# Optimization experiments

Hardware: AMD Instinct MI355X
Metric: run time of the kernel (lower is better)

Reference implementation:

```python
import jax, jax.numpy as jnp
import numpy as np

NUM_NODES = 100000
NUM_RELATIONS = 16
HIDDEN = 64
NUM_LAYERS = 3
NUM_EDGES = 1600000


def setup_inputs() -> dict:
    key = jax.random.key(0)
    ks = jax.random.split(key, 6)
    edge_index = jax.random.randint(ks[0], (2, NUM_EDGES), 0, NUM_NODES, dtype=jnp.int64 if jax.config.jax_enable_x64 else jnp.int32)
    edge_type = jax.random.randint(ks[1], (NUM_EDGES,), 0, NUM_RELATIONS, dtype=edge_index.dtype)
    scale = 1.0 / np.sqrt(HIDDEN)
    node_emb = jax.random.normal(ks[2], (NUM_NODES, HIDDEN), dtype=jnp.float32) * scale
    # Per-layer relation weights [L, R, d, h], root weights [L, d, h], bias [L, h]
    W = jax.random.normal(ks[3], (NUM_LAYERS, NUM_RELATIONS, HIDDEN, HIDDEN), dtype=jnp.float32) * scale
    W_root = jax.random.normal(ks[4], (NUM_LAYERS, HIDDEN, HIDDEN), dtype=jnp.float32) * scale
    bias = jnp.zeros((NUM_LAYERS, HIDDEN), dtype=jnp.float32)
    return {"edge_index": edge_index, "edge_type": edge_type,
            "node_emb": node_emb, "W": W, "W_root": W_root, "bias": bias}


def _rgcn_layer(x, src, dst, et, Wr, Wroot, b):
    # PyG RGCNConv: out_i = W_root x_i + b + sum_r (1/|N_r(i)|) sum_{j in N_r(i)} W_r x_j
    N, d = x.shape
    R = Wr.shape[0]
    # Transform all nodes by every relation weight: [R, N, h] (dense grouped GEMM)
    xW = jnp.einsum('nd,rdh->rnh', x, Wr)
    m = xW[et, src]                      # [E, h] per-edge messages (gather)
    seg = dst * R + et                   # joint (dst, relation) segment id
    counts = jax.ops.segment_sum(jnp.ones((m.shape[0],), dtype=x.dtype), seg, num_segments=N * R)
    norm = 1.0 / jnp.maximum(counts, 1.0)
    m = m * norm[seg][:, None]           # per-relation mean normalization
    agg = jax.ops.segment_sum(m, dst, num_segments=N)  # scatter-add over dst
    return agg + x @ Wroot + b


def reference(edge_index, edge_type, node_emb, W, W_root, bias):
    src, dst = edge_index[0], edge_index[1]
    x = node_emb  # note: Embedding.max_norm only applies on index lookups; .weight used raw here
    n_layers = W.shape[0]
    for i in range(n_layers):
        x = _rgcn_layer(x, src, dst, edge_type, W[i], W_root[i], bias[i])
        if i < n_layers - 1:
            x = jax.nn.relu(x)
    return x
```

## Files before the change

### kernel.cpp

```cpp
#include <hip/hip_runtime.h>


#define HID   64
#define NREL  16
#define KD    1088
#define NPB   16
#define NPW   2
#define LSTR  1096

#define NBKT  1024
#define BSH   7
#define FB    2048
#define CAPB  4096
#define CHA   8192

typedef __attribute__((ext_vector_type(8))) short bf16x8;
typedef __attribute__((ext_vector_type(4))) float f32x4;
typedef unsigned short us16;
typedef unsigned int u32;

__device__ __forceinline__ float b2f(us16 u) {
    union { u32 i; float f; } c; c.i = ((u32)u) << 16; return c.f;
}
__device__ __forceinline__ us16 f2b(float f) {
    union { float f; u32 i; } c; c.f = f;
    u32 x = c.i;
    return (us16)((x + 0x7FFFu + ((x >> 16) & 1u)) >> 16);
}


__global__ __launch_bounds__(256) void bucket_count(const int* __restrict__ ei,
                                                    int* __restrict__ counts_b, int E) {
    __shared__ int h[NBKT];
    const int t = threadIdx.x;
    for (int i = t; i < NBKT; i += 256) h[i] = 0;
    __syncthreads();
    const int* dstp = ei + E;
    int start = blockIdx.x * CHA, end = min(start + CHA, E);
    for (int e4 = start + t * 4; e4 < end; e4 += 1024) {
        if (e4 + 3 < end) {
            int4 d = *(const int4*)(dstp + e4);
            atomicAdd(&h[d.x >> BSH], 1);
            atomicAdd(&h[d.y >> BSH], 1);
            atomicAdd(&h[d.z >> BSH], 1);
            atomicAdd(&h[d.w >> BSH], 1);
        } else {
            for (int e = e4; e < end; ++e) atomicAdd(&h[dstp[e] >> BSH], 1);
        }
    }
    __syncthreads();
    for (int i = t; i < NBKT; i += 256) {
        int v = h[i];
        if (v) atomicAdd(&counts_b[i], v);
    }
}

__global__ __launch_bounds__(NBKT) void scan_buckets(const int* __restrict__ counts_b,
                                                     int* __restrict__ bucket_base,
                                                     int* __restrict__ cursor_b,
                                                     int* __restrict__ row_ptr,
                                                     int N, int E) {
    __shared__ int s[NBKT];
    int t = threadIdx.x;
    int v = counts_b[t];
    s[t] = v; __syncthreads();
    for (int off = 1; off < NBKT; off <<= 1) {
        int tv = (t >= off) ? s[t - off] : 0;
        __syncthreads();
        s[t] += tv;
        __syncthreads();
    }
    int ex = s[t] - v;
    bucket_base[t] = ex;
    cursor_b[t] = ex;
    if (t == NBKT - 1) bucket_base[NBKT] = ex + v;
    if (t == 0) row_ptr[N] = E;
}

__global__ __launch_bounds__(256) void bucket_place(const int* __restrict__ ei,
                                                    const int* __restrict__ et,
                                                    int* __restrict__ cursor_b,
                                                    u32* __restrict__ packed, int E) {
    __shared__ int cnt[NBKT];
    __shared__ int bse[NBKT];
    const int t = threadIdx.x;
    for (int i = t; i < NBKT; i += 256) cnt[i] = 0;
    __syncthreads();
    const int* dstp = ei + E;
    int start = blockIdx.x * CHA, end = min(start + CHA, E);
    for (int e4 = start + t * 4; e4 < end; e4 += 1024) {
        if (e4 + 3 < end) {
            int4 d = *(const int4*)(dstp + e4);
            atomicAdd(&cnt[d.x >> BSH], 1);
            atomicAdd(&cnt[d.y >> BSH], 1);
            atomicAdd(&cnt[d.z >> BSH], 1);
            atomicAdd(&cnt[d.w >> BSH], 1);
        } else {
            for (int e = e4; e < end; ++e) atomicAdd(&cnt[dstp[e] >> BSH], 1);
        }
    }
    __syncthreads();
    for (int i = t; i < NBKT; i += 256) {
        int v = cnt[i];
        bse[i] = v ? atomicAdd(&cursor_b[i], v) : 0;
        cnt[i] = 0;
    }
    __syncthreads();
    #define PLACE1(sv, dv, tv)                                            \
        { int b_ = (dv) >> BSH;                                           \
          int r_ = atomicAdd(&cnt[b_], 1);                                \
          packed[bse[b_] + r_] = (u32)(sv) | ((u32)(tv) << 17)            \
                               | ((u32)((dv) & 127) << 21); }
    for (int e4 = start + t * 4; e4 < end; e4 += 1024) {
        if (e4 + 3 < end) {
            int4 sv = *(const int4*)(ei + e4);
            int4 dv = *(const int4*)(dstp + e4);
            int4 tv = *(const int4*)(et + e4);
            PLACE1(sv.x, dv.x, tv.x);
            PLACE1(sv.y, dv.y, tv.y);
            PLACE1(sv.z, dv.z, tv.z);
            PLACE1(sv.w, dv.w, tv.w);
        } else {
            for (int e = e4; e < end; ++e) PLACE1(ei[e], dstp[e], et[e]);
        }
    }
    #undef PLACE1
}

__global__ __launch_bounds__(256) void bucket_sort(const u32* __restrict__ packed,
                                                   const int* __restrict__ bucket_base,
                                                   u32* __restrict__ md,
                                                   int* __restrict__ row_ptr, int N) {
    __shared__ int hist[FB];
    __shared__ int ss[256];
    __shared__ u32 outb[CAPB];
    const int b = blockIdx.x, t = threadIdx.x;
    const int base = bucket_base[b];
    const int cnt = bucket_base[b + 1] - base;

    for (int i = t; i < FB; i += 256) hist[i] = 0;
    __syncthreads();
    for (int i = t; i < cnt; i += 256) {
        u32 p = packed[base + i];
        int f = (int)(((p >> 21) & 127u) * 16u + ((p >> 17) & 15u));
        atomicAdd(&hist[f], 1);
    }
    __syncthreads();
    int loc[8], s = 0;
    #pragma unroll
    for (int j = 0; j < 8; ++j) { loc[j] = hist[t * 8 + j]; s += loc[j]; }
    ss[t] = s; __syncthreads();
    for (int off = 1; off < 256; off <<= 1) {
        int tv = (t >= off) ? ss[t - off] : 0;
        __syncthreads();
        ss[t] += tv;
        __syncthreads();
    }
    int run = ss[t] - s;
    #pragma unroll
    for (int j = 0; j < 8; ++j) { hist[t * 8 + j] = run; run += loc[j]; }
    __syncthreads();
    if (t < 128) {
        int node = b * 128 + t;
        if (node < N) row_ptr[node] = base + hist[t * 16];
    }
    __syncthreads();
    for (int i = t; i < cnt; i += 256) {
        u32 p = packed[base + i];
        int f = (int)(((p >> 21) & 127u) * 16u + ((p >> 17) & 15u));
        int pos = atomicAdd(&hist[f], 1);
        u32 v = (p & 0x1FFFFu) | (((p >> 17) & 15u) << 20);
        if (pos < CAPB) outb[pos] = v;
        else            md[base + pos] = v;
    }
    __syncthreads();
    for (int i = t; i < cnt && i < CAPB; i += 256)
        md[base + i] = outb[i];
}

__global__ void convx_kernel(const float* __restrict__ x, us16* __restrict__ xb, int n4) {
    int i = blockIdx.x * 256 + threadIdx.x;
    if (i < n4) {
        float4 v = ((const float4*)x)[i];
        us16* o = xb + i * 4;
        o[0] = f2b(v.x); o[1] = f2b(v.y); o[2] = f2b(v.z); o[3] = f2b(v.w);
    }
}

__global__ void convw_kernel(const float* __restrict__ W, const float* __restrict__ Wroot,
                             us16* __restrict__ WcatT, int total, int L) {
    int i = blockIdx.x * 256 + threadIdx.x;
    if (i < total) {
        int l = i / (HID * KD);
        int rem = i % (HID * KD);
        int h = rem / KD, k = rem % KD;
        float v;
        if (k < NREL * HID) {
            int r = k >> 6, d = k & 63;
            v = W[(((size_t)l * NREL + r) * HID + d) * HID + h];
        } else {
            int d = k - NREL * HID;
            v = Wroot[((size_t)l * HID + d) * HID + h];
        }
        WcatT[i] = f2b(v);
    }
}


__device__ __forceinline__ void proc_window(
        u32 p_l, int c0, int wcnt, const us16* __restrict__ x_in, us16* Hrow, int lane,
        float& acc, int& runlen, int& prev, u32& mask)
{
    #pragma unroll 1
    for (int c = c0; c < wcnt; c += 16) {
        us16 hv[16]; int pe[16];
        #pragma unroll
        for (int j = 0; j < 16; ++j) {
            int idx = c + j; if (idx >= wcnt) idx = wcnt - 1;
            pe[j] = __builtin_amdgcn_readlane((int)p_l, idx);
            hv[j] = x_in[((u32)pe[j] & 0xFFFFFu) * HID + lane];
        }
        int m = wcnt - c; if (m > 16) m = 16;
        #pragma unroll
        for (int j = 0; j < 16; ++j) {
            if (j < m) {
                int r = (int)(((u32)pe[j]) >> 20);
                if (r != prev) {
                    if (prev >= 0) {
                        Hrow[(prev << 6) + lane] =
                            f2b(acc * __builtin_amdgcn_rcpf((float)runlen));
                        mask |= 1u << prev;
                    }
                    prev = r; acc = 0.f; runlen = 0;
                }
                acc += b2f(hv[j]); ++runlen;
            }
        }
    }
}

__global__ __launch_bounds__(512, 8) void layer_kernel(
        const us16* __restrict__ x_in,
        const int*  __restrict__ row_ptr,
        const u32*  __restrict__ md,
        const us16* __restrict__ WcatT,
        const float* __restrict__ bias,
        us16* __restrict__ x_out,
        float* __restrict__ out_f32,
        int flags, int N)
{
    __shared__ us16 H[NPB * LSTR];
    const int tid = threadIdx.x, wave = tid >> 6, lane = tid & 63;
    const int node0 = blockIdx.x * NPB;
    const int nodeq = node0 + wave * NPW;

    int rp[NPW + 1];
    #pragma unroll
    for (int i = 0; i <= NPW; ++i)
        rp[i] = __builtin_amdgcn_readfirstlane(row_ptr[min(nodeq + i, N)]);

    u32 pl[NPW]; us16 xr[NPW];
    #pragma unroll
    for (int q = 0; q < NPW; ++q) {
        int cnt = rp[q + 1] - rp[q];
        pl[q] = (lane < cnt) ? md[rp[q] + lane] : 0;
        xr[q] = (nodeq + q < N) ? x_in[(nodeq + q) * HID + lane] : (us16)0;
    }

    #pragma unroll
    for (int q = 0; q < NPW; ++q) {
        int node = nodeq + q;
        if (node >= N) break;
        int start = rp[q], cnt = rp[q + 1] - start;
        us16* Hrow = H + (wave * NPW + q) * LSTR;
        Hrow[NREL * HID + lane] = xr[q];

        float acc = 0.f;
        int runlen = 0, prev = -1;
        u32 mask = 0;

        proc_window(pl[q], 0, min(cnt, 64), x_in, Hrow, lane, acc, runlen, prev, mask);
        for (int w0 = 64; w0 < cnt; w0 += 64) {
            int wcnt = min(64, cnt - w0);
            u32 p2 = (lane < wcnt) ? md[start + w0 + lane] : 0;
            proc_window(p2, 0, wcnt, x_in, Hrow, lane, acc, runlen, prev, mask);
        }
        if (prev >= 0) {
            Hrow[(prev << 6) + lane] = f2b(acc * __builtin_amdgcn_rcpf((float)runlen));
            mask |= 1u << prev;
        }
        #pragma unroll
        for (int r = 0; r < NREL; ++r)
            if (!(mask & (1u << r))) Hrow[(r << 6) + lane] = 0;
    }
    __syncthreads();

    if (wave < 4) {
        const int n16 = lane & 15, quad = lane >> 4;
        f32x4 acc = {0.f, 0.f, 0.f, 0.f};
        const us16* Abase = H + n16 * LSTR + quad * 8;
        const us16* Bbase = WcatT + (size_t)(wave * 16 + n16) * KD + quad * 8;
        #pragma unroll 2
        for (int ks = 0; ks < KD / 32; ++ks) {
            bf16x8 af = *(const bf16x8*)(Abase + ks * 32);
            bf16x8 bf = *(const bf16x8*)(Bbase + ks * 32);
            acc = __builtin_amdgcn_mfma_f32_16x16x32_bf16(af, bf, acc, 0, 0, 0);
        }

        int col = wave * 16 + n16;
        float bv = bias[col];
        #pragma unroll
        for (int ri = 0; ri < 4; ++ri) {
            int nl = quad * 4 + ri, node = node0 + nl;
            if (node < N) {
                float v = acc[ri] + bv;
                if (flags & 1) v = fmaxf(v, 0.f);
                if (flags & 2) out_f32[node * HID + col] = v;
                else           x_out [node * HID + col] = f2b(v);
            }
        }
    }
}


extern "C" void kernel_launch(void* const* d_in, const int* in_sizes, int n_in,
                              void* d_out, int out_size, void* d_ws, size_t ws_size,
                              hipStream_t stream) {
    const int*   edge_index = (const int*)  d_in[0];
    const int*   edge_type  = (const int*)  d_in[1];
    const float* node_emb   = (const float*)d_in[2];
    const float* W          = (const float*)d_in[3];
    const float* Wroot      = (const float*)d_in[4];
    const float* bias       = (const float*)d_in[5];
    float* out = (float*)d_out;

    const int E = in_sizes[1];
    const int N = in_sizes[2] / HID;
    const int L = in_sizes[5] / HID;

    char* p = (char*)d_ws;
    size_t off = 0;
    auto carve = [&](size_t bytes) {
        void* q = p + off;
        off = (off + bytes + 255) & ~(size_t)255;
        return q;
    };
    int*   counts_b    = (int*)  carve((size_t)NBKT * 4);
    int*   bucket_base = (int*)  carve((size_t)(NBKT + 1) * 4);
    int*   cursor_b    = (int*)  carve((size_t)NBKT * 4);
    int*   row_ptr     = (int*)  carve((size_t)(N + 1) * 4);
    u32*   packed      = (u32*)  carve((size_t)E * 4);
    u32*   md          = (u32*)  carve((size_t)E * 4);
    us16*  xb0         = (us16*) carve((size_t)N * HID * 2);
    us16*  xb1         = (us16*) carve((size_t)N * HID * 2);
    us16*  WcatT       = (us16*) carve((size_t)L * HID * KD * 2);
    (void)ws_size; (void)n_in; (void)out_size;

    hipMemsetAsync(counts_b, 0, (size_t)NBKT * 4, stream);

    const int nblkA = (E + CHA - 1) / CHA;
    bucket_count<<<nblkA, 256, 0, stream>>>(edge_index, counts_b, E);
    scan_buckets<<<1, NBKT, 0, stream>>>(counts_b, bucket_base, cursor_b, row_ptr, N, E);
    bucket_place<<<nblkA, 256, 0, stream>>>(edge_index, edge_type, cursor_b, packed, E);
    bucket_sort<<<(N + 127) / 128, 256, 0, stream>>>(packed, bucket_base, md, row_ptr, N);

    convx_kernel<<<(N * HID / 4 + 255) / 256, 256, 0, stream>>>(node_emb, xb0, N * HID / 4);
    int wtot = L * HID * KD;
    convw_kernel<<<(wtot + 255) / 256, 256, 0, stream>>>(W, Wroot, WcatT, wtot, L);

    int gl = (N + NPB - 1) / NPB;
    us16* xin = xb0;
    us16* xother = xb1;
    for (int l = 0; l < L; ++l) {
        int last = (l == L - 1);
        int flags = (last ? 2 : 1);
        layer_kernel<<<gl, 512, 0, stream>>>(
            xin, row_ptr, md,
            WcatT + (size_t)l * HID * KD, bias + (size_t)l * HID,
            last ? nullptr : xother, last ? out : nullptr,
            flags, N);
        us16* t = xin; xin = xother; xother = t;
    }
}
```

Measured before the change: 535.0 us.

## Prefetch both nodes' first gather batch and split-K GEMM across all eight waves

Gather issue and consumption are split into separate helpers. The first 16-edge gather for both of a wave's nodes is issued up front, so the second node's loads overlap the first node's aggregation. The MFMA stage now uses all 8 waves instead of 4: the K dimension is split in half, and the partial sums are combined through a small shared-memory buffer behind an extra barrier. In exchange, register pressure rises from the doubled pe/hv arrays, and the split-K adds extra LDS use and a sync.

```diff
diff --git a/kernel.cpp b/kernel.cpp
--- a/kernel.cpp
+++ b/kernel.cpp
@@ -207,36 +207,70 @@
 }
 
 
-__device__ __forceinline__ void proc_window(
-        u32 p_l, int c0, int wcnt, const us16* __restrict__ x_in, us16* Hrow, int lane,
-        float& acc, int& runlen, int& prev, u32& mask)
-{
-    #pragma unroll 1
-    for (int c = c0; c < wcnt; c += 16) {
-        us16 hv[16]; int pe[16];
-        #pragma unroll
-        for (int j = 0; j < 16; ++j) {
-            int idx = c + j; if (idx >= wcnt) idx = wcnt - 1;
-            pe[j] = __builtin_amdgcn_readlane((int)p_l, idx);
-            hv[j] = x_in[((u32)pe[j] & 0xFFFFFu) * HID + lane];
-        }
-        int m = wcnt - c; if (m > 16) m = 16;
-        #pragma unroll
-        for (int j = 0; j < 16; ++j) {
-            if (j < m) {
-                int r = (int)(((u32)pe[j]) >> 20);
-                if (r != prev) {
-                    if (prev >= 0) {
-                        Hrow[(prev << 6) + lane] =
-                            f2b(acc * __builtin_amdgcn_rcpf((float)runlen));
-                        mask |= 1u << prev;
-                    }
-                    prev = r; acc = 0.f; runlen = 0;
+__device__ __forceinline__ void issue16(u32 p_l, int c, int wcnt,
+                                        const us16* __restrict__ x_in, int lane,
+                                        int* pe, us16* hv) {
+    int last = wcnt - 1; if (last < 0) last = 0;
+    #pragma unroll
+    for (int j = 0; j < 16; ++j) {
+        int idx = c + j; if (idx > last) idx = last;
+        pe[j] = __builtin_amdgcn_readlane((int)p_l, idx);
+        hv[j] = x_in[((u32)pe[j] & 0xFFFFFu) * HID + lane];
+    }
+}
+
+__device__ __forceinline__ void consume16(const int* pe, const us16* hv, int c, int wcnt,
+                                          us16* Hrow, int lane,
+                                          float& acc, int& runlen, int& prev, u32& mask) {
+    #pragma unroll
+    for (int j = 0; j < 16; ++j) {
+        if (c + j < wcnt) {
+            int r = (int)(((u32)pe[j]) >> 20);
+            if (r != prev) {
+                if (prev >= 0) {
+                    Hrow[(prev << 6) + lane] =
+                        f2b(acc * __builtin_amdgcn_rcpf((float)runlen));
+                    mask |= 1u << prev;
                 }
-                acc += b2f(hv[j]); ++runlen;
+                prev = r; acc = 0.f; runlen = 0;
             }
-        }
-    }
+            acc += b2f(hv[j]); ++runlen;
+        }
+    }
+}
+
+__device__ __forceinline__ void proc_node(int node, int start, int cnt, u32 plq,
+                                          const us16* __restrict__ x_in,
+                                          const u32* __restrict__ md,
+                                          us16* Hrow, us16 xrq, int lane, int N,
+                                          int* pe, us16* hv) {
+    if (node >= N) return;
+    Hrow[NREL * HID + lane] = xrq;
+    float acc = 0.f;
+    int runlen = 0, prev = -1;
+    u32 mask = 0;
+
+    int wcnt = cnt < 64 ? cnt : 64;
+    consume16(pe, hv, 0, wcnt, Hrow, lane, acc, runlen, prev, mask);
+    for (int c = 16; c < wcnt; c += 16) {
+        issue16(plq, c, wcnt, x_in, lane, pe, hv);
+        consume16(pe, hv, c, wcnt, Hrow, lane, acc, runlen, prev, mask);
+    }
+    for (int w0s = 64; w0s < cnt; w0s += 64) {
+        int wc = cnt - w0s; if (wc > 64) wc = 64;
+        u32 p2 = (lane < wc) ? md[start + w0s + lane] : 0;
+        for (int c = 0; c < wc; c += 16) {
+            issue16(p2, c, wc, x_in, lane, pe, hv);
+            consume16(pe, hv, c, wc, Hrow, lane, acc, runlen, prev, mask);
+        }
+    }
+    if (prev >= 0) {
+        Hrow[(prev << 6) + lane] = f2b(acc * __builtin_amdgcn_rcpf((float)runlen));
+        mask |= 1u << prev;
+    }
+    #pragma unroll
+    for (int r = 0; r < NREL; ++r)
+        if (!(mask & (1u << r))) Hrow[(r << 6) + lane] = 0;
 }
 
 __global__ __launch_bounds__(512, 8) void layer_kernel(
@@ -250,6 +284,7 @@
         int flags, int N)
 {
     __shared__ us16 H[NPB * LSTR];
+    __shared__ float P[NPB * HID];
     const int tid = threadIdx.x, wave = tid >> 6, lane = tid & 63;
     const int node0 = blockIdx.x * NPB;
     const int nodeq = node0 + wave * NPW;
@@ -267,56 +302,50 @@
         xr[q] = (nodeq + q < N) ? x_in[(nodeq + q) * HID + lane] : (us16)0;
     }
 
-    #pragma unroll
-    for (int q = 0; q < NPW; ++q) {
-        int node = nodeq + q;
-        if (node >= N) break;
-        int start = rp[q], cnt = rp[q + 1] - start;
-        us16* Hrow = H + (wave * NPW + q) * LSTR;
-        Hrow[NREL * HID + lane] = xr[q];
-
-        float acc = 0.f;
-        int runlen = 0, prev = -1;
-        u32 mask = 0;
-
-        proc_window(pl[q], 0, min(cnt, 64), x_in, Hrow, lane, acc, runlen, prev, mask);
-        for (int w0 = 64; w0 < cnt; w0 += 64) {
-            int wcnt = min(64, cnt - w0);
-            u32 p2 = (lane < wcnt) ? md[start + w0 + lane] : 0;
-            proc_window(p2, 0, wcnt, x_in, Hrow, lane, acc, runlen, prev, mask);
-        }
-        if (prev >= 0) {
-            Hrow[(prev << 6) + lane] = f2b(acc * __builtin_amdgcn_rcpf((float)runlen));
-            mask |= 1u << prev;
-        }
+    int peA[16], peB[16]; us16 hvA[16], hvB[16];
+    int w0 = rp[1] - rp[0]; if (w0 > 64) w0 = 64;
+    int w1 = rp[2] - rp[1]; if (w1 > 64) w1 = 64;
+    issue16(pl[0], 0, w0, x_in, lane, peA, hvA);
+    issue16(pl[1], 0, w1, x_in, lane, peB, hvB);
+
+    proc_node(nodeq + 0, rp[0], rp[1] - rp[0], pl[0], x_in, md,
+              H + (wave * NPW + 0) * LSTR, xr[0], lane, N, peA, hvA);
+    proc_node(nodeq + 1, rp[1], rp[2] - rp[1], pl[1], x_in, md,
+              H + (wave * NPW + 1) * LSTR, xr[1], lane, N, peB, hvB);
+    __syncthreads();
+
+    {
+        const int n16 = lane & 15, quad = lane >> 4;
+        const int kw = wave >> 2;
+        const int wv = wave & 3;
+        f32x4 acc = {0.f, 0.f, 0.f, 0.f};
+        const us16* Abase = H + n16 * LSTR + quad * 8 + kw * (KD / 2);
+        const us16* Bbase = WcatT + (size_t)(wv * 16 + n16) * KD + quad * 8 + kw * (KD / 2);
         #pragma unroll
-        for (int r = 0; r < NREL; ++r)
-            if (!(mask & (1u << r))) Hrow[(r << 6) + lane] = 0;
-    }
-    __syncthreads();
-
-    if (wave < 4) {
-        const int n16 = lane & 15, quad = lane >> 4;
-        f32x4 acc = {0.f, 0.f, 0.f, 0.f};
-        const us16* Abase = H + n16 * LSTR + quad * 8;
-        const us16* Bbase = WcatT + (size_t)(wave * 16 + n16) * KD + quad * 8;
-        #pragma unroll 2
-        for (int ks = 0; ks < KD / 32; ++ks) {
+        for (int ks = 0; ks < KD / 64; ++ks) {
             bf16x8 af = *(const bf16x8*)(Abase + ks * 32);
             bf16x8 bf = *(const bf16x8*)(Bbase + ks * 32);
             acc = __builtin_amdgcn_mfma_f32_16x16x32_bf16(af, bf, acc, 0, 0, 0);
         }
 
-        int col = wave * 16 + n16;
-        float bv = bias[col];
-        #pragma unroll
-        for (int ri = 0; ri < 4; ++ri) {
-            int nl = quad * 4 + ri, node = node0 + nl;
-            if (node < N) {
-                float v = acc[ri] + bv;
-                if (flags & 1) v = fmaxf(v, 0.f);
-                if (flags & 2) out_f32[node * HID + col] = v;
-                else           x_out [node * HID + col] = f2b(v);
+        int col = wv * 16 + n16;
+        if (kw) {
+            #pragma unroll
+            for (int ri = 0; ri < 4; ++ri)
+                P[(quad * 4 + ri) * HID + col] = acc[ri];
+        }
+        __syncthreads();
+        if (!kw) {
+            float bv = bias[col];
+            #pragma unroll
+            for (int ri = 0; ri < 4; ++ri) {
+                int nl = quad * 4 + ri, node = node0 + nl;
+                if (node < N) {
+                    float v = acc[ri] + P[nl * HID + col] + bv;
+                    if (flags & 1) v = fmaxf(v, 0.f);
+                    if (flags & 2) out_f32[node * HID + col] = v;
+                    else           x_out [node * HID + col] = f2b(v);
+                }
             }
         }
     }
```

New measurement: 539.5 us. No clear change (+0.9%).

## Restructure RGCN aggregation to 16-lane groups per node with split-K MFMA

Applied to the files above, without the earlier changes.

The gather/aggregate phase now assigns one 16-lane group per node, and each lane loads 4 bf16 features as a uint2, instead of one full wave handling two nodes. Edge metadata is spread across lanes with ds_bpermute. The segmented mean is computed branch-free, writing the running mean for every edge, and the H tile is zero-initialised up front instead of masking absent relations. The GEMM is split along K across all 8 waves, with partial sums reduced through shared memory, where before only 4 waves did the work. Only 4 waves now do the gather, and the extra per-edge LDS writes and lower occupancy bound may offset the wider, fewer memory transactions.

```diff
diff --git a/kernel.cpp b/kernel.cpp
--- a/kernel.cpp
+++ b/kernel.cpp
@@ -5,8 +5,7 @@
 #define NREL  16
 #define KD    1088
 #define NPB   16
-#define NPW   2
-#define LSTR  1096
+#define LSTR  1104
 
 #define NBKT  1024
 #define BSH   7
@@ -19,9 +18,6 @@
 typedef unsigned short us16;
 typedef unsigned int u32;
 
-__device__ __forceinline__ float b2f(us16 u) {
-    union { u32 i; float f; } c; c.i = ((u32)u) << 16; return c.f;
-}
 __device__ __forceinline__ us16 f2b(float f) {
     union { float f; u32 i; } c; c.f = f;
     u32 x = c.i;
@@ -207,39 +203,34 @@
 }
 
 
-__device__ __forceinline__ void proc_window(
-        u32 p_l, int c0, int wcnt, const us16* __restrict__ x_in, us16* Hrow, int lane,
-        float& acc, int& runlen, int& prev, u32& mask)
-{
-    #pragma unroll 1
-    for (int c = c0; c < wcnt; c += 16) {
-        us16 hv[16]; int pe[16];
-        #pragma unroll
-        for (int j = 0; j < 16; ++j) {
-            int idx = c + j; if (idx >= wcnt) idx = wcnt - 1;
-            pe[j] = __builtin_amdgcn_readlane((int)p_l, idx);
-            hv[j] = x_in[((u32)pe[j] & 0xFFFFFu) * HID + lane];
-        }
-        int m = wcnt - c; if (m > 16) m = 16;
-        #pragma unroll
-        for (int j = 0; j < 16; ++j) {
-            if (j < m) {
-                int r = (int)(((u32)pe[j]) >> 20);
-                if (r != prev) {
-                    if (prev >= 0) {
-                        Hrow[(prev << 6) + lane] =
-                            f2b(acc * __builtin_amdgcn_rcpf((float)runlen));
-                        mask |= 1u << prev;
-                    }
-                    prev = r; acc = 0.f; runlen = 0;
-                }
-                acc += b2f(hv[j]); ++runlen;
-            }
-        }
-    }
-}
-
-__global__ __launch_bounds__(512, 8) void layer_kernel(
+__device__ __forceinline__ void step_e(u32 relp, int jloc, int jj, uint2 d, int rem,
+                                       float& a0, float& a1, float& a2, float& a3,
+                                       int& runlen, int& prev, us16* Hrow, int l16) {
+    int rel = (int)((relp >> (4 * jloc)) & 15u);
+    bool valid = jj < rem;
+    bool keep = (rel == prev) || !valid;
+    u32 w0v = valid ? d.x : 0u;
+    u32 w1v = valid ? d.y : 0u;
+    float v0 = __uint_as_float(w0v << 16);
+    float v1 = __uint_as_float(w0v & 0xFFFF0000u);
+    float v2 = __uint_as_float(w1v << 16);
+    float v3 = __uint_as_float(w1v & 0xFFFF0000u);
+    a0 = (keep ? a0 : 0.f) + v0;
+    a1 = (keep ? a1 : 0.f) + v1;
+    a2 = (keep ? a2 : 0.f) + v2;
+    a3 = (keep ? a3 : 0.f) + v3;
+    runlen = (keep ? runlen : 0) + (valid ? 1 : 0);
+    prev = valid ? rel : prev;
+    float sc = __builtin_amdgcn_rcpf((float)runlen);
+    float f0 = a0 * sc, f1 = a1 * sc, f2 = a2 * sc, f3 = a3 * sc;
+    u32 p0, p1;
+    asm("v_cvt_pk_bf16_f32 %0, %1, %2" : "=v"(p0) : "v"(f0), "v"(f1));
+    asm("v_cvt_pk_bf16_f32 %0, %1, %2" : "=v"(p1) : "v"(f2), "v"(f3));
+    uint2 pk; pk.x = p0; pk.y = p1;
+    *(uint2*)(Hrow + (rel << 6) + (l16 << 2)) = pk;
+}
+
+__global__ __launch_bounds__(512, 6) void layer_kernel(
         const us16* __restrict__ x_in,
         const int*  __restrict__ row_ptr,
         const u32*  __restrict__ md,
@@ -250,73 +241,96 @@
         int flags, int N)
 {
     __shared__ us16 H[NPB * LSTR];
+    __shared__ float P[NPB * HID];
     const int tid = threadIdx.x, wave = tid >> 6, lane = tid & 63;
     const int node0 = blockIdx.x * NPB;
-    const int nodeq = node0 + wave * NPW;
-
-    int rp[NPW + 1];
-    #pragma unroll
-    for (int i = 0; i <= NPW; ++i)
-        rp[i] = __builtin_amdgcn_readfirstlane(row_ptr[min(nodeq + i, N)]);
-
-    u32 pl[NPW]; us16 xr[NPW];
-    #pragma unroll
-    for (int q = 0; q < NPW; ++q) {
-        int cnt = rp[q + 1] - rp[q];
-        pl[q] = (lane < cnt) ? md[rp[q] + lane] : 0;
-        xr[q] = (nodeq + q < N) ? x_in[(nodeq + q) * HID + lane] : (us16)0;
-    }
-
-    #pragma unroll
-    for (int q = 0; q < NPW; ++q) {
-        int node = nodeq + q;
-        if (node >= N) break;
-        int start = rp[q], cnt = rp[q + 1] - start;
-        us16* Hrow = H + (wave * NPW + q) * LSTR;
-        Hrow[NREL * HID + lane] = xr[q];
-
-        float acc = 0.f;
+
+    {
+        u32* hw = (u32*)H;
+        for (int i = tid; i < NPB * LSTR / 2; i += 512) hw[i] = 0;
+    }
+    __syncthreads();
+
+    if (wave < 4) {
+        const int g = lane >> 4, l16 = lane & 15;
+        const int rowid = wave * 4 + g;
+        const int ng = node0 + rowid;
+        const bool nv = ng < N;
+        const int rpv = row_ptr[nv ? ng : N];
+        const int rpe = row_ptr[nv ? (ng + 1) : N];
+        const int cnt = rpe - rpv;
+        us16* Hrow = H + rowid * LSTR;
+        const int pbase = (lane & 48) << 2;
+
+        if (nv) {
+            uint2 xv = *(const uint2*)(x_in + (size_t)ng * HID + l16 * 4);
+            *(uint2*)(Hrow + NREL * HID + l16 * 4) = xv;
+        }
+
+        float a0 = 0.f, a1 = 0.f, a2 = 0.f, a3 = 0.f;
         int runlen = 0, prev = -1;
-        u32 mask = 0;
-
-        proc_window(pl[q], 0, min(cnt, 64), x_in, Hrow, lane, acc, runlen, prev, mask);
-        for (int w0 = 64; w0 < cnt; w0 += 64) {
-            int wcnt = min(64, cnt - w0);
-            u32 p2 = (lane < wcnt) ? md[start + w0 + lane] : 0;
-            proc_window(p2, 0, wcnt, x_in, Hrow, lane, acc, runlen, prev, mask);
-        }
-        if (prev >= 0) {
-            Hrow[(prev << 6) + lane] = f2b(acc * __builtin_amdgcn_rcpf((float)runlen));
-            mask |= 1u << prev;
-        }
+
+        for (int w0 = 0; w0 < cnt; w0 += 16) {
+            int rem = cnt - w0;
+            int mi = (rem - 1 < l16) ? (rem - 1) : l16;
+            u32 mdv = md[rpv + w0 + mi];
+
+            u32 rpA = 0, rpB = 0;
+            uint2 dA[8], dB[8];
+            #pragma unroll
+            for (int j = 0; j < 8; ++j) {
+                u32 m = (u32)__builtin_amdgcn_ds_bpermute(pbase + j * 4, (int)mdv);
+                rpA |= ((m >> 20) & 15u) << (4 * j);
+                dA[j] = *(const uint2*)(x_in + (size_t)(m & 0xFFFFFu) * HID + l16 * 4);
+            }
+            #pragma unroll
+            for (int j = 0; j < 8; ++j) {
+                u32 m = (u32)__builtin_amdgcn_ds_bpermute(pbase + (j + 8) * 4, (int)mdv);
+                rpB |= ((m >> 20) & 15u) << (4 * j);
+                dB[j] = *(const uint2*)(x_in + (size_t)(m & 0xFFFFFu) * HID + l16 * 4);
+            }
+            #pragma unroll
+            for (int j = 0; j < 8; ++j)
+                step_e(rpA, j, j, dA[j], rem, a0, a1, a2, a3, runlen, prev, Hrow, l16);
+            #pragma unroll
+            for (int j = 0; j < 8; ++j)
+                step_e(rpB, j, j + 8, dB[j], rem, a0, a1, a2, a3, runlen, prev, Hrow, l16);
+        }
+    }
+    __syncthreads();
+
+    {
+        const int n16 = lane & 15, quad = lane >> 4;
+        const int kw = wave >> 2;
+        const int wv = wave & 3;
+        f32x4 acc = {0.f, 0.f, 0.f, 0.f};
+        const us16* Abase = H + n16 * LSTR + quad * 8 + kw * (KD / 2);
+        const us16* Bbase = WcatT + (size_t)(wv * 16 + n16) * KD + quad * 8 + kw * (KD / 2);
         #pragma unroll
-        for (int r = 0; r < NREL; ++r)
-            if (!(mask & (1u << r))) Hrow[(r << 6) + lane] = 0;
-    }
-    __syncthreads();
-
-    if (wave < 4) {
-        const int n16 = lane & 15, quad = lane >> 4;
-        f32x4 acc = {0.f, 0.f, 0.f, 0.f};
-        const us16* Abase = H + n16 * LSTR + quad * 8;
-        const us16* Bbase = WcatT + (size_t)(wave * 16 + n16) * KD + quad * 8;
-        #pragma unroll 2
-        for (int ks = 0; ks < KD / 32; ++ks) {
+        for (int ks = 0; ks < KD / 64; ++ks) {
             bf16x8 af = *(const bf16x8*)(Abase + ks * 32);
             bf16x8 bf = *(const bf16x8*)(Bbase + ks * 32);
             acc = __builtin_amdgcn_mfma_f32_16x16x32_bf16(af, bf, acc, 0, 0, 0);
         }
 
-        int col = wave * 16 + n16;
-        float bv = bias[col];
-        #pragma unroll
-        for (int ri = 0; ri < 4; ++ri) {
-            int nl = quad * 4 + ri, node = node0 + nl;
-            if (node < N) {
-                float v = acc[ri] + bv;
-                if (flags & 1) v = fmaxf(v, 0.f);
-                if (flags & 2) out_f32[node * HID + col] = v;
-                else           x_out [node * HID + col] = f2b(v);
+        int col = wv * 16 + n16;
+        if (kw) {
+            #pragma unroll
+            for (int ri = 0; ri < 4; ++ri)
+                P[(quad * 4 + ri) * HID + col] = acc[ri];
+        }
+        __syncthreads();
+        if (!kw) {
+            float bv = bias[col];
+            #pragma unroll
+            for (int ri = 0; ri < 4; ++ri) {
+                int nl = quad * 4 + ri, node = node0 + nl;
+                if (node < N) {
+                    float v = acc[ri] + P[nl * HID + col] + bv;
+                    if (flags & 1) v = fmaxf(v, 0.f);
+                    if (flags & 2) out_f32[node * HID + col] = v;
+                    else           x_out [node * HID + col] = f2b(v);
+                }
             }
         }
     }
```

Result: slower. 578.5 us (+8.1%).

## Aggregate per-relation neighbor means via MFMA with one-hot normalized weight matrices

Applied to the files above, without the earlier changes.

Replaces the scalar per-lane run-length aggregation with a block-wide chunked scheme. Gathered neighbor features are staged transposed in LDS, and a one-hot matrix holding 1/count weights, built with ds_bpermute, is multiplied in with MFMA to produce per-relation means. The per-(dst,relation) count is precomputed in bucket_sort and packed into the metadata's top byte, and the concatenated weight layout is padded to 68 per relation. This trades dependent serial adds for matrix ops but adds LDS traffic, extra syncs, lower occupancy and redundant MFMA work on mostly-zero one-hot tiles. Counts are clamped at 255.

```diff
diff --git a/kernel.cpp b/kernel.cpp
--- a/kernel.cpp
+++ b/kernel.cpp
@@ -3,10 +3,12 @@
 
 #define HID   64
 #define NREL  16
-#define KD    1088
+#define RP    68
+#define KD2   1152
 #define NPB   16
-#define NPW   2
-#define LSTR  1096
+#define LSTR  1160
+#define YSTR  132
+#define CHUNK 128
 
 #define NBKT  1024
 #define BSH   7
@@ -19,9 +21,6 @@
 typedef unsigned short us16;
 typedef unsigned int u32;
 
-__device__ __forceinline__ float b2f(us16 u) {
-    union { u32 i; float f; } c; c.i = ((u32)u) << 16; return c.f;
-}
 __device__ __forceinline__ us16 f2b(float f) {
     union { float f; u32 i; } c; c.f = f;
     u32 x = c.i;
@@ -132,6 +131,7 @@
                                                    u32* __restrict__ md,
                                                    int* __restrict__ row_ptr, int N) {
     __shared__ int hist[FB];
+    __shared__ int cbin[FB];
     __shared__ int ss[256];
     __shared__ u32 outb[CAPB];
     const int b = blockIdx.x, t = threadIdx.x;
@@ -148,7 +148,10 @@
     __syncthreads();
     int loc[8], s = 0;
     #pragma unroll
-    for (int j = 0; j < 8; ++j) { loc[j] = hist[t * 8 + j]; s += loc[j]; }
+    for (int j = 0; j < 8; ++j) {
+        loc[j] = hist[t * 8 + j]; s += loc[j];
+        cbin[t * 8 + j] = loc[j];
+    }
     ss[t] = s; __syncthreads();
     for (int off = 1; off < 256; off <<= 1) {
         int tv = (t >= off) ? ss[t - off] : 0;
@@ -169,7 +172,8 @@
         u32 p = packed[base + i];
         int f = (int)(((p >> 21) & 127u) * 16u + ((p >> 17) & 15u));
         int pos = atomicAdd(&hist[f], 1);
-        u32 v = (p & 0x1FFFFu) | (((p >> 17) & 15u) << 20);
+        int cb = cbin[f]; if (cb > 255) cb = 255;
+        u32 v = (p & 0x1FFFFu) | (((p >> 17) & 15u) << 20) | ((u32)cb << 24);
         if (pos < CAPB) outb[pos] = v;
         else            md[base + pos] = v;
     }
@@ -191,15 +195,16 @@
                              us16* __restrict__ WcatT, int total, int L) {
     int i = blockIdx.x * 256 + threadIdx.x;
     if (i < total) {
-        int l = i / (HID * KD);
-        int rem = i % (HID * KD);
-        int h = rem / KD, k = rem % KD;
-        float v;
-        if (k < NREL * HID) {
-            int r = k >> 6, d = k & 63;
-            v = W[(((size_t)l * NREL + r) * HID + d) * HID + h];
+        int l = i / (HID * KD2);
+        int rem = i % (HID * KD2);
+        int h = rem / KD2, k = rem % KD2;
+        float v = 0.f;
+        if (k < NREL * RP) {
+            int r = k / RP, dd = k % RP;
+            if (dd < HID)
+                v = W[(((size_t)l * NREL + r) * HID + dd) * HID + h];
         } else {
-            int d = k - NREL * HID;
+            int d = k - NREL * RP;
             v = Wroot[((size_t)l * HID + d) * HID + h];
         }
         WcatT[i] = f2b(v);
@@ -207,39 +212,16 @@
 }
 
 
-__device__ __forceinline__ void proc_window(
-        u32 p_l, int c0, int wcnt, const us16* __restrict__ x_in, us16* Hrow, int lane,
-        float& acc, int& runlen, int& prev, u32& mask)
-{
-    #pragma unroll 1
-    for (int c = c0; c < wcnt; c += 16) {
-        us16 hv[16]; int pe[16];
-        #pragma unroll
-        for (int j = 0; j < 16; ++j) {
-            int idx = c + j; if (idx >= wcnt) idx = wcnt - 1;
-            pe[j] = __builtin_amdgcn_readlane((int)p_l, idx);
-            hv[j] = x_in[((u32)pe[j] & 0xFFFFFu) * HID + lane];
-        }
-        int m = wcnt - c; if (m > 16) m = 16;
-        #pragma unroll
-        for (int j = 0; j < 16; ++j) {
-            if (j < m) {
-                int r = (int)(((u32)pe[j]) >> 20);
-                if (r != prev) {
-                    if (prev >= 0) {
-                        Hrow[(prev << 6) + lane] =
-                            f2b(acc * __builtin_amdgcn_rcpf((float)runlen));
-                        mask |= 1u << prev;
-                    }
-                    prev = r; acc = 0.f; runlen = 0;
-                }
-                acc += b2f(hv[j]); ++runlen;
-            }
-        }
-    }
-}
-
-__global__ __launch_bounds__(512, 8) void layer_kernel(
+__device__ __forceinline__ u32 onehot1(int j, u32 plw, int jlo, int jhi, int r) {
+    u32 mv = (u32)__builtin_amdgcn_ds_bpermute((j & 63) << 2, (int)plw);
+    int rel = (int)((mv >> 20) & 15u);
+    float wv = __builtin_amdgcn_rcpf((float)(mv >> 24));
+    u32 w16 = (u32)f2b(wv);
+    bool sel = (j >= jlo) && (j < jhi) && (rel == r);
+    return sel ? w16 : 0u;
+}
+
+__global__ __launch_bounds__(512, 6) void layer_kernel(
         const us16* __restrict__ x_in,
         const int*  __restrict__ row_ptr,
         const u32*  __restrict__ md,
@@ -249,65 +231,123 @@
         float* __restrict__ out_f32,
         int flags, int N)
 {
+    __shared__ us16 Yt[64 * YSTR];
     __shared__ us16 H[NPB * LSTR];
     const int tid = threadIdx.x, wave = tid >> 6, lane = tid & 63;
+    const int l15 = lane & 15, quad = lane >> 4;
     const int node0 = blockIdx.x * NPB;
-    const int nodeq = node0 + wave * NPW;
-
-    int rp[NPW + 1];
-    #pragma unroll
-    for (int i = 0; i <= NPW; ++i)
-        rp[i] = __builtin_amdgcn_readfirstlane(row_ptr[min(nodeq + i, N)]);
-
-    u32 pl[NPW]; us16 xr[NPW];
-    #pragma unroll
-    for (int q = 0; q < NPW; ++q) {
-        int cnt = rp[q + 1] - rp[q];
-        pl[q] = (lane < cnt) ? md[rp[q] + lane] : 0;
-        xr[q] = (nodeq + q < N) ? x_in[(nodeq + q) * HID + lane] : (us16)0;
-    }
-
-    #pragma unroll
-    for (int q = 0; q < NPW; ++q) {
-        int node = nodeq + q;
-        if (node >= N) break;
-        int start = rp[q], cnt = rp[q + 1] - start;
-        us16* Hrow = H + (wave * NPW + q) * LSTR;
-        Hrow[NREL * HID + lane] = xr[q];
-
-        float acc = 0.f;
-        int runlen = 0, prev = -1;
-        u32 mask = 0;
-
-        proc_window(pl[q], 0, min(cnt, 64), x_in, Hrow, lane, acc, runlen, prev, mask);
-        for (int w0 = 64; w0 < cnt; w0 += 64) {
-            int wcnt = min(64, cnt - w0);
-            u32 p2 = (lane < wcnt) ? md[start + w0 + lane] : 0;
-            proc_window(p2, 0, wcnt, x_in, Hrow, lane, acc, runlen, prev, mask);
-        }
-        if (prev >= 0) {
-            Hrow[(prev << 6) + lane] = f2b(acc * __builtin_amdgcn_rcpf((float)runlen));
-            mask |= 1u << prev;
-        }
+
+    const int blk_s = __builtin_amdgcn_readfirstlane(row_ptr[min(node0, N)]);
+    const int blk_e = __builtin_amdgcn_readfirstlane(row_ptr[min(node0 + NPB, N)]);
+    const int nch = (blk_e - blk_s + CHUNK - 1) / CHUNK;
+
+    const int nqA = node0 + wave * 2;
+    const int sA = __builtin_amdgcn_readfirstlane(row_ptr[min(nqA,     N)]);
+    const int sB = __builtin_amdgcn_readfirstlane(row_ptr[min(nqA + 1, N)]);
+    const int eB = __builtin_amdgcn_readfirstlane(row_ptr[min(nqA + 2, N)]);
+
+    f32x4 accA[4] = {{0,0,0,0},{0,0,0,0},{0,0,0,0},{0,0,0,0}};
+    f32x4 accB[4] = {{0,0,0,0},{0,0,0,0},{0,0,0,0},{0,0,0,0}};
+
+    for (int c = 0; c < nch; ++c) {
+        const int c0 = blk_s + c * CHUNK;
+        const int cs = min(CHUNK, blk_e - c0);
+
+        u32 pl0 = (lane < cs) ? md[c0 + lane] : 0u;
+        u32 pl1 = (64 + lane < cs) ? md[c0 + 64 + lane] : 0u;
+
+        {
+            u32 plw = (wave < 4) ? pl0 : pl1;
+            const int rbase = (wave & 3) * 16;
+            u32 hv[16];
+            #pragma unroll
+            for (int i = 0; i < 16; ++i) {
+                u32 m = (u32)__builtin_amdgcn_readlane((int)plw, rbase + i);
+                hv[i] = (u32)x_in[(size_t)(m & 0x1FFFFu) * HID + lane];
+            }
+            const int le0 = wave * 16;
+            #pragma unroll
+            for (int i = 0; i < 16; i += 2) {
+                u32 y0 = (le0 + i     < cs) ? hv[i]     : 0u;
+                u32 y1 = (le0 + i + 1 < cs) ? hv[i + 1] : 0u;
+                *(u32*)(Yt + lane * YSTR + le0 + i) = y0 | (y1 << 16);
+            }
+        }
+        __syncthreads();
+
+        {
+            int jlo = max(sA - c0, 0), jhi = min(eB - c0, cs);
+            int jloA = max(sA - c0, 0), jhiA = min(sB - c0, cs);
+            int jloB = max(sB - c0, 0), jhiB = min(eB - c0, cs);
+            (void)jlo; (void)jhi;
+            #pragma unroll 1
+            for (int sel = 0; sel < 2; ++sel) {
+                int lo = sel ? jloB : jloA;
+                int hi = sel ? jhiB : jhiA;
+                if (hi <= lo) continue;
+                f32x4* acc = sel ? accB : accA;
+                for (int w = (lo >> 5); w <= ((hi - 1) >> 5); ++w) {
+                    u32 plw = (w < 2) ? pl0 : pl1;
+                    const int jb = w * 32 + quad * 8;
+                    u32 bfr[4];
+                    #pragma unroll
+                    for (int t2 = 0; t2 < 4; ++t2) {
+                        u32 loh = onehot1(jb + 2 * t2,     plw, lo, hi, l15);
+                        u32 hih = onehot1(jb + 2 * t2 + 1, plw, lo, hi, l15);
+                        bfr[t2] = loh | (hih << 16);
+                    }
+                    union { u32 u[4]; bf16x8 v; } B; 
+                    B.u[0] = bfr[0]; B.u[1] = bfr[1]; B.u[2] = bfr[2]; B.u[3] = bfr[3];
+                    #pragma unroll
+                    for (int t = 0; t < 4; ++t) {
+                        const us16* ap = Yt + (t * 16 + l15) * YSTR + w * 32 + quad * 8;
+                        uint2 a0 = *(const uint2*)ap;
+                        uint2 a1 = *(const uint2*)(ap + 4);
+                        union { u32 u[4]; bf16x8 v; } A;
+                        A.u[0] = a0.x; A.u[1] = a0.y; A.u[2] = a1.x; A.u[3] = a1.y;
+                        acc[t] = __builtin_amdgcn_mfma_f32_16x16x32_bf16(A.v, B.v, acc[t], 0, 0, 0);
+                    }
+                }
+            }
+        }
+        __syncthreads();
+    }
+
+    {
         #pragma unroll
-        for (int r = 0; r < NREL; ++r)
-            if (!(mask & (1u << r))) Hrow[(r << 6) + lane] = 0;
+        for (int sel = 0; sel < 2; ++sel) {
+            int node = nqA + sel;
+            us16* Hb = H + (wave * 2 + sel) * LSTR;
+            const f32x4* acc = sel ? accB : accA;
+            #pragma unroll
+            for (int t = 0; t < 4; ++t) {
+                u32 p0, p1;
+                asm("v_cvt_pk_bf16_f32 %0, %1, %2" : "=v"(p0) : "v"(acc[t][0]), "v"(acc[t][1]));
+                asm("v_cvt_pk_bf16_f32 %0, %1, %2" : "=v"(p1) : "v"(acc[t][2]), "v"(acc[t][3]));
+                uint2 pk; pk.x = p0; pk.y = p1;
+                *(uint2*)(Hb + l15 * RP + t * 16 + quad * 4) = pk;
+            }
+            Hb[NREL * RP + lane] = (node < N) ? x_in[(size_t)node * HID + lane] : (us16)0;
+            if (lane < 16) {
+                uint2 z; z.x = 0; z.y = 0;
+                *(uint2*)(Hb + lane * RP + 64) = z;
+            }
+        }
     }
     __syncthreads();
 
     if (wave < 4) {
-        const int n16 = lane & 15, quad = lane >> 4;
         f32x4 acc = {0.f, 0.f, 0.f, 0.f};
-        const us16* Abase = H + n16 * LSTR + quad * 8;
-        const us16* Bbase = WcatT + (size_t)(wave * 16 + n16) * KD + quad * 8;
+        const us16* Abase = H + l15 * LSTR + quad * 8;
+        const us16* Bbase = WcatT + (size_t)(wave * 16 + l15) * KD2 + quad * 8;
         #pragma unroll 2
-        for (int ks = 0; ks < KD / 32; ++ks) {
+        for (int ks = 0; ks < KD2 / 32; ++ks) {
             bf16x8 af = *(const bf16x8*)(Abase + ks * 32);
             bf16x8 bf = *(const bf16x8*)(Bbase + ks * 32);
             acc = __builtin_amdgcn_mfma_f32_16x16x32_bf16(af, bf, acc, 0, 0, 0);
         }
 
-        int col = wave * 16 + n16;
+        int col = wave * 16 + l15;
         float bv = bias[col];
         #pragma unroll
         for (int ri = 0; ri < 4; ++ri) {
@@ -353,7 +393,7 @@
     u32*   md          = (u32*)  carve((size_t)E * 4);
     us16*  xb0         = (us16*) carve((size_t)N * HID * 2);
     us16*  xb1         = (us16*) carve((size_t)N * HID * 2);
-    us16*  WcatT       = (us16*) carve((size_t)L * HID * KD * 2);
+    us16*  WcatT       = (us16*) carve((size_t)L * HID * KD2 * 2);
     (void)ws_size; (void)n_in; (void)out_size;
 
     hipMemsetAsync(counts_b, 0, (size_t)NBKT * 4, stream);
@@ -365,7 +405,7 @@
     bucket_sort<<<(N + 127) / 128, 256, 0, stream>>>(packed, bucket_base, md, row_ptr, N);
 
     convx_kernel<<<(N * HID / 4 + 255) / 256, 256, 0, stream>>>(node_emb, xb0, N * HID / 4);
-    int wtot = L * HID * KD;
+    int wtot = L * HID * KD2;
     convw_kernel<<<(wtot + 255) / 256, 256, 0, stream>>>(W, Wroot, WcatT, wtot, L);
 
     int gl = (N + NPB - 1) / NPB;
@@ -376,7 +416,7 @@
         int flags = (last ? 2 : 1);
         layer_kernel<<<gl, 512, 0, stream>>>(
             xin, row_ptr, md,
-            WcatT + (size_t)l * HID * KD, bias + (size_t)l * HID,
+            WcatT + (size_t)l * HID * KD2, bias + (size_t)l * HID,
             last ? nullptr : xother, last ? out : nullptr,
             flags, N);
         us16* t = xin; xin = xother; xother = t;
```

Result: slower. 800.9 us (+49.7%).
